# Kernel optimization log

Hardware: AMD Instinct MI355X
Metric: run time of the kernel (lower is better)

## Reference

```python
import jax, jax.numpy as jnp
import numpy as np

NEG_SLOPE = 0.2  # PyG GATv2Conv default negative_slope


def _gatv2(h, src, dst, Wl, bl, Wr, br, att, bias, N):
    """GATv2Conv (concat=True). h: [N,Fin]; att: [H,F]; returns [N,H*F]."""
    H, F = att.shape
    xl = (h @ Wl + bl).reshape(N, H, F)  # source transform
    xr = (h @ Wr + br).reshape(N, H, F)  # target transform
    # per-edge GATv2 score: a^T LeakyReLU(xl[src] + xr[dst])
    e = jax.nn.leaky_relu(xl[src] + xr[dst], negative_slope=NEG_SLOPE)  # [E,H,F]
    logits = jnp.einsum('ehf,hf->eh', e, att)  # [E,H]
    # segment softmax over destination nodes (self-loops guarantee nonempty segments)
    m = jax.ops.segment_max(logits, dst, num_segments=N)  # [N,H]
    p = jnp.exp(logits - m[dst])
    s = jax.ops.segment_sum(p, dst, num_segments=N)  # [N,H]
    alpha = p / s[dst]  # [E,H]
    out = jax.ops.segment_sum(alpha[:, :, None] * xl[src], dst, num_segments=N)  # [N,H,F]
    return out.reshape(N, H * F) + bias


def setup_inputs() -> dict:
    key = jax.random.key(0)
    ks = jax.random.split(key, 16)
    N, E = 30000, 480000
    L, D, H, F = 50, 100, 3, 100
    W = D * H  # 300
    sc = 0.1  # keep activations stable through 5 layers
    return {
        'x': jax.random.randint(ks[0], (N,), 0, L),
        'edge_index': jax.random.randint(ks[1], (2, E), 0, N),
        'emb': jax.random.normal(ks[2], (L, D), jnp.float32),
        'Wl0': jax.random.normal(ks[3], (D, W), jnp.float32) * sc,
        'bl0': jnp.zeros((W,), jnp.float32),
        'Wr0': jax.random.normal(ks[4], (D, W), jnp.float32) * sc,
        'br0': jnp.zeros((W,), jnp.float32),
        'att0': jax.random.normal(ks[5], (H, F), jnp.float32) * sc,
        'bias0': jnp.zeros((W,), jnp.float32),
        'Wl': jax.random.normal(ks[6], (4, W, W), jnp.float32) * sc,
        'bl': jnp.zeros((4, W), jnp.float32),
        'Wr': jax.random.normal(ks[7], (4, W, W), jnp.float32) * sc,
        'br': jnp.zeros((4, W), jnp.float32),
        'att': jax.random.normal(ks[8], (4, H, F), jnp.float32) * sc,
        'bias': jnp.zeros((4, W), jnp.float32),
    }


def reference(x, edge_index, emb, Wl0, bl0, Wr0, br0, att0, bias0,
              Wl, bl, Wr, br, att, bias):
    N = x.shape[0]
    loops = jnp.arange(N)
    src = jnp.concatenate([edge_index[0], loops])  # PyG add_self_loops=True
    dst = jnp.concatenate([edge_index[1], loops])
    h = emb[x]  # node_embedding(x).squeeze()
    h = jax.nn.relu(_gatv2(h, src, dst, Wl0, bl0, Wr0, br0, att0, bias0, N))
    for i in range(4):  # remaining num_gnn_layers-1 convs, each followed by ReLU
        h = jax.nn.relu(_gatv2(h, src, dst, Wl[i], bl[i], Wr[i], br[i], att[i], bias[i], N))
    return h  # [N, heads*hidden] = [N, 300]
```

## Files before the change

kernel.cpp:

```cpp
#include <hip/hip_runtime.h>

#define NODES   30000
#define E0N     480000
#define ETOT    510000
#define D0      100
#define WDIM    300
#define NW      600
#define NEG     0.2f
#define XLP     320

typedef __bf16 bf16x8 __attribute__((ext_vector_type(8)));
typedef float  f32x4  __attribute__((ext_vector_type(4)));

__global__ void count_edges(const int* __restrict__ ei, int* __restrict__ counts) {
    int e = blockIdx.x * 256 + threadIdx.x;
    if (e >= ETOT) return;
    int d = (e < E0N) ? ei[E0N + e] : (e - E0N);
    atomicAdd(&counts[d], 1);
}

__global__ __launch_bounds__(1024) void scan_kernel(const int* __restrict__ counts,
                                                    int* __restrict__ offsets, int n) {
    __shared__ int lds[1024];
    const int CH = 32;
    int t = threadIdx.x;
    int base = t * CH;
    int loc[CH];
    int sum = 0;
    #pragma unroll
    for (int i = 0; i < CH; i++) {
        int v = (base + i < n) ? counts[base + i] : 0;
        loc[i] = sum;
        sum += v;
    }
    lds[t] = sum;
    __syncthreads();
    for (int off = 1; off < 1024; off <<= 1) {
        int v = (t >= off) ? lds[t - off] : 0;
        __syncthreads();
        lds[t] += v;
        __syncthreads();
    }
    int ex = (t == 0) ? 0 : lds[t - 1];
    #pragma unroll
    for (int i = 0; i < CH; i++) {
        int idx = base + i;
        if (idx < n) offsets[idx] = ex + loc[i];
    }
    if (t == 0) offsets[n] = lds[1023];
}

__global__ void scatter_edges(const int* __restrict__ ei, const int* __restrict__ offsets,
                              int* __restrict__ cursor, int* __restrict__ csr_src) {
    int e = blockIdx.x * 256 + threadIdx.x;
    if (e >= ETOT) return;
    int s, d;
    if (e < E0N) { s = ei[e]; d = ei[E0N + e]; }
    else         { s = e - E0N; d = s; }
    int pos = offsets[d] + atomicAdd(&cursor[d], 1);
    csr_src[pos] = s;
}

__device__ __forceinline__ void bfrag_one(const float* Bl, const float* Br,
                                          bf16x8* out, int K, int t) {
    int lane = t & 63;
    int n16  = (t >> 6) % 40;
    int s    = t / (64 * 40);
    int c = n16 * 16 + (lane & 15);
    union { bf16x8 v; __bf16 e[8]; } hi, lo;
    #pragma unroll
    for (int j = 0; j < 8; j++) {
        int k = s * 32 + ((lane >> 4) * 8) + j;
        float x = 0.f;
        if (k < K && c < NW)
            x = (c < WDIM) ? Bl[(size_t)k * WDIM + c] : Br[(size_t)k * WDIM + c - WDIM];
        __bf16 h = (__bf16)x;
        hi.e[j] = h;
        lo.e[j] = (__bf16)(x - (float)h);
    }
    size_t base = ((size_t)(s * 40 + n16) * 2) * 64 + lane;
    out[base]      = hi.v;
    out[base + 64] = lo.v;
}

__global__ void make_bfrag_all(const float* __restrict__ Wl0, const float* __restrict__ Wr0,
                               const float* __restrict__ Wl, const float* __restrict__ Wr,
                               bf16x8* __restrict__ frag0, bf16x8* __restrict__ frag1,
                               size_t fragstride) {
    int t = blockIdx.x * 256 + threadIdx.x;
    const int L0 = 4 * 40 * 64, LN = 10 * 40 * 64;
    if (t < L0) {
        bfrag_one(Wl0, Wr0, frag0, D0, t);
    } else {
        int u = t - L0;
        int layer = u / LN;
        if (layer >= 4) return;
        bfrag_one(Wl + (size_t)layer * WDIM * WDIM, Wr + (size_t)layer * WDIM * WDIM,
                  frag1 + layer * fragstride, WDIM, u - layer * LN);
    }
}

__global__ __launch_bounds__(256) void gemm_mfma(
    const float* __restrict__ A, const int* __restrict__ xmap, int use_map,
    const bf16x8* __restrict__ Bfrag,
    const float* __restrict__ bl, const float* __restrict__ br,
    ushort* __restrict__ Cl16, float* __restrict__ Cr,
    int M, int K, int ksteps) {

    __shared__ bf16x8 Alds[8][2][64];
    __shared__ bf16x8 Blds[8][2][64];

    int id = blockIdx.x;
    int mb = (id & 7) + 8 * (id / 40);
    int cb = (id >> 3) % 5;
    if (mb >= 235) return;

    int tid  = threadIdx.x;
    int lane = tid & 63;
    int wid  = tid >> 6;
    int wm = wid >> 1, wn = wid & 1;
    int row0 = mb * 128;

    f32x4 acc[4][4] = {};

    for (int s = 0; s < ksteps; s++) {
        int kt = s * 32;
        #pragma unroll
        for (int u0 = 0; u0 < 2; u0++) {
            int u = u0 * 256 + tid;
            int m16  = u >> 6;
            int slot = u & 63;
            int kh = slot >> 4, rl = slot & 15;
            int gr = row0 + m16 * 16 + rl;
            int gc = kt + kh * 8;
            float4 v0 = make_float4(0.f,0.f,0.f,0.f), v1 = v0;
            if (gr < M) {
                int ar = use_map ? xmap[gr] : gr;
                const float* ap = A + (size_t)ar * K + gc;
                if (gc + 4 <= K) v0 = *(const float4*)ap;
                if (gc + 8 <= K) v1 = *(const float4*)(ap + 4);
            }
            union { bf16x8 v; __bf16 e[8]; } hi, lo;
            const float* xs0 = (const float*)&v0;
            const float* xs1 = (const float*)&v1;
            #pragma unroll
            for (int j = 0; j < 8; j++) {
                float x = (j < 4) ? xs0[j] : xs1[j - 4];
                __bf16 h = (__bf16)x;
                hi.e[j] = h;
                lo.e[j] = (__bf16)(x - (float)h);
            }
            Alds[m16][0][slot] = hi.v;
            Alds[m16][1][slot] = lo.v;
        }
        {
            const float4* bsrc = (const float4*)(Bfrag + ((size_t)(s * 40 + cb * 8) * 2) * 64);
            float4* bdst = (float4*)&Blds[0][0][0];
            #pragma unroll
            for (int c = 0; c < 4; c++)
                bdst[c * 256 + tid] = bsrc[c * 256 + tid];
        }
        __syncthreads();

        bf16x8 af[4][2], bfr[4][2];
        #pragma unroll
        for (int m = 0; m < 4; m++) {
            af[m][0] = Alds[wm * 4 + m][0][lane];
            af[m][1] = Alds[wm * 4 + m][1][lane];
        }
        #pragma unroll
        for (int n = 0; n < 4; n++) {
            bfr[n][0] = Blds[wn * 4 + n][0][lane];
            bfr[n][1] = Blds[wn * 4 + n][1][lane];
        }
        #pragma unroll
        for (int m = 0; m < 4; m++)
            #pragma unroll
            for (int n = 0; n < 4; n++) {
                acc[m][n] = __builtin_amdgcn_mfma_f32_16x16x32_bf16(af[m][1], bfr[n][0], acc[m][n], 0, 0, 0);
                acc[m][n] = __builtin_amdgcn_mfma_f32_16x16x32_bf16(af[m][0], bfr[n][1], acc[m][n], 0, 0, 0);
                acc[m][n] = __builtin_amdgcn_mfma_f32_16x16x32_bf16(af[m][0], bfr[n][0], acc[m][n], 0, 0, 0);
            }
        __syncthreads();
    }

    int r0 = row0 + wm * 64;
    int c0 = cb * 128 + wn * 64;
    #pragma unroll
    for (int m = 0; m < 4; m++)
        #pragma unroll
        for (int n = 0; n < 4; n++) {
            #pragma unroll
            for (int reg = 0; reg < 4; reg++) {
                int gr = r0 + m * 16 + (lane >> 4) * 4 + reg;
                int gc = c0 + n * 16 + (lane & 15);
                if (gr < M && gc < NW) {
                    if (gc < WDIM) {
                        float v = acc[m][n][reg] + bl[gc];
                        __bf16 b = (__bf16)v;
                        Cl16[(size_t)gr * XLP + gc] = *(ushort*)&b;
                    } else {
                        int cc = gc - WDIM;
                        Cr[(size_t)gr * WDIM + cc] = acc[m][n][reg] + br[cc];
                    }
                }
            }
        }
}

__global__ __launch_bounds__(256) void gat_edge_agg(
    const ushort* __restrict__ xl, const float* __restrict__ xr,
    const int* __restrict__ offsets, const int* __restrict__ csr_src,
    const float* __restrict__ att, const float* __restrict__ bias,
    float* __restrict__ fout) {
    __shared__ float st[4][64][8];
    int wid  = threadIdx.x >> 6;
    int lane = threadIdx.x & 63;
    int node = blockIdx.x * 2 + (wid >> 1);
    int sub  = wid & 1;
    int r = lane & 3;
    bool c0 = lane < 50;
    bool c1 = lane < 36;

    float2 aw2[3], xr2[3];
    const float2* xrrow = (const float2*)(xr + (size_t)node * WDIM);
    #pragma unroll
    for (int j = 0; j < 3; j++) {
        int i = lane + 64 * j;
        if (i < 150) {
            aw2[j].x = att[2 * i]; aw2[j].y = att[2 * i + 1];
            xr2[j] = xrrow[i];
        } else {
            aw2[j].x = 0.f; aw2[j].y = 0.f;
            xr2[j].x = 0.f; xr2[j].y = 0.f;
        }
    }

    float mq = -1e38f, sq = 0.f;
    float2 acc2[3] = {};

    int beg = offsets[node], end = offsets[node + 1];
    int half = (end - beg + 1) >> 1;
    int lo = beg + sub * half;
    int hi = sub ? end : beg + half;

    for (int i = lo; i < hi; i += 2) {
        bool act_b = (i + 1) < hi;
        int sa = csr_src[i];
        int sb = csr_src[act_b ? i + 1 : i];
        const ushort* ra = xl + (size_t)sa * XLP;
        const ushort* rb = xl + (size_t)sb * XLP;
        ushort2 ua[3], ub[3];
        ua[0] = *(const ushort2*)(ra + 2 * lane);
        ub[0] = *(const ushort2*)(rb + 2 * lane);
        ua[1] = *(const ushort2*)(ra + 2 * (lane + 64));
        ub[1] = *(const ushort2*)(rb + 2 * (lane + 64));
        if (lane < 32) {
            ua[2] = *(const ushort2*)(ra + 2 * (lane + 128));
            ub[2] = *(const ushort2*)(rb + 2 * (lane + 128));
        } else { ua[2].x = ua[2].y = ub[2].x = ub[2].y = 0; }

        float2 va[3], vb[3];
        #pragma unroll
        for (int j = 0; j < 3; j++) {
            va[j].x = __uint_as_float(((unsigned)ua[j].x) << 16);
            va[j].y = __uint_as_float(((unsigned)ua[j].y) << 16);
            vb[j].x = __uint_as_float(((unsigned)ub[j].x) << 16);
            vb[j].y = __uint_as_float(((unsigned)ub[j].y) << 16);
        }

        float qa[3], qb[3];
        #pragma unroll
        for (int j = 0; j < 3; j++) {
            float tax = va[j].x + xr2[j].x; tax = fmaxf(tax, NEG * tax);
            float tay = va[j].y + xr2[j].y; tay = fmaxf(tay, NEG * tay);
            float tbx = vb[j].x + xr2[j].x; tbx = fmaxf(tbx, NEG * tbx);
            float tby = vb[j].y + xr2[j].y; tby = fmaxf(tby, NEG * tby);
            qa[j] = tax * aw2[j].x + tay * aw2[j].y;
            qb[j] = tbx * aw2[j].x + tby * aw2[j].y;
        }
        float pa0 = c0 ? qa[0] : 0.f;
        float pa1 = (c0 ? 0.f : qa[0]) + (c1 ? qa[1] : 0.f);
        float pa2 = (c1 ? 0.f : qa[1]) + qa[2];
        float pb0 = c0 ? qb[0] : 0.f;
        float pb1 = (c0 ? 0.f : qb[0]) + (c1 ? qb[1] : 0.f);
        float pb2 = (c1 ? 0.f : qb[1]) + qb[2];

        pa0 += __shfl_xor(pa0, 1, 64); pa1 += __shfl_xor(pa1, 1, 64); pa2 += __shfl_xor(pa2, 1, 64);
        pb0 += __shfl_xor(pb0, 1, 64); pb1 += __shfl_xor(pb1, 1, 64); pb2 += __shfl_xor(pb2, 1, 64);
        pa0 += __shfl_xor(pa0, 2, 64); pa1 += __shfl_xor(pa1, 2, 64); pa2 += __shfl_xor(pa2, 2, 64);
        pb0 += __shfl_xor(pb0, 2, 64); pb1 += __shfl_xor(pb1, 2, 64); pb2 += __shfl_xor(pb2, 2, 64);
        float sqa = (r == 1) ? pa1 : ((r == 2) ? pa2 : pa0);
        float sqb = (r == 1) ? pb1 : ((r == 2) ? pb2 : pb0);
        sqa += __shfl_xor(sqa, 4, 64);  sqb += __shfl_xor(sqb, 4, 64);
        sqa += __shfl_xor(sqa, 8, 64);  sqb += __shfl_xor(sqb, 8, 64);
        sqa += __shfl_xor(sqa, 16, 64); sqb += __shfl_xor(sqb, 16, 64);
        sqa += __shfl_xor(sqa, 32, 64); sqb += __shfl_xor(sqb, 32, 64);
        if (!act_b) sqb = -3e38f;

        float hiq = fmaxf(sqa, sqb);
        if (__any(hiq > mq + 8.f)) {
            float nmq = fmaxf(mq, hiq);
            float eq = __expf(mq - nmq);
            sq *= eq;
            float e0 = __shfl(eq, 0, 64), e1 = __shfl(eq, 1, 64), e2 = __shfl(eq, 2, 64);
            float ej0 = c0 ? e0 : e1, ej1 = c1 ? e1 : e2;
            acc2[0].x *= ej0; acc2[0].y *= ej0;
            acc2[1].x *= ej1; acc2[1].y *= ej1;
            acc2[2].x *= e2;  acc2[2].y *= e2;
            mq = nmq;
        }
        float cqa = __expf(sqa - mq), cqb = __expf(sqb - mq);
        sq += cqa + cqb;
        float ca0 = __shfl(cqa, 0, 64), ca1 = __shfl(cqa, 1, 64), ca2 = __shfl(cqa, 2, 64);
        float cb0 = __shfl(cqb, 0, 64), cb1 = __shfl(cqb, 1, 64), cb2 = __shfl(cqb, 2, 64);
        float caj[3] = { c0 ? ca0 : ca1, c1 ? ca1 : ca2, ca2 };
        float cbj[3] = { c0 ? cb0 : cb1, c1 ? cb1 : cb2, cb2 };
        #pragma unroll
        for (int j = 0; j < 3; j++) {
            acc2[j].x = fmaf(caj[j], va[j].x, acc2[j].x);
            acc2[j].y = fmaf(caj[j], va[j].y, acc2[j].y);
            acc2[j].x = fmaf(cbj[j], vb[j].x, acc2[j].x);
            acc2[j].y = fmaf(cbj[j], vb[j].y, acc2[j].y);
        }
    }

    st[wid][lane][0] = mq;
    st[wid][lane][1] = sq;
    st[wid][lane][2] = acc2[0].x; st[wid][lane][3] = acc2[0].y;
    st[wid][lane][4] = acc2[1].x; st[wid][lane][5] = acc2[1].y;
    st[wid][lane][6] = acc2[2].x; st[wid][lane][7] = acc2[2].y;
    __syncthreads();
    if (sub) return;

    float m1 = st[wid ^ 1][lane][0];
    float s1 = st[wid ^ 1][lane][1];
    float2 o1[3];
    o1[0].x = st[wid ^ 1][lane][2]; o1[0].y = st[wid ^ 1][lane][3];
    o1[1].x = st[wid ^ 1][lane][4]; o1[1].y = st[wid ^ 1][lane][5];
    o1[2].x = st[wid ^ 1][lane][6]; o1[2].y = st[wid ^ 1][lane][7];

    float M  = fmaxf(mq, m1);
    float ea = __expf(mq - M), eb = __expf(m1 - M);
    float sF = sq * ea + s1 * eb;
    float iq = 1.f / sF;
    float ea0 = __shfl(ea, 0, 64), ea1 = __shfl(ea, 1, 64), ea2 = __shfl(ea, 2, 64);
    float eb0 = __shfl(eb, 0, 64), eb1 = __shfl(eb, 1, 64), eb2 = __shfl(eb, 2, 64);
    float i0  = __shfl(iq, 0, 64), i1  = __shfl(iq, 1, 64), i2  = __shfl(iq, 2, 64);
    float eaj[3]  = { c0 ? ea0 : ea1, c1 ? ea1 : ea2, ea2 };
    float ebj[3]  = { c0 ? eb0 : eb1, c1 ? eb1 : eb2, eb2 };
    float isel[3] = { c0 ? i0 : i1,  c1 ? i1 : i2,  i2 };

    #pragma unroll
    for (int j = 0; j < 3; j++) {
        int fi = lane + 64 * j;
        if (fi < 150) {
            float ax = acc2[j].x * eaj[j] + o1[j].x * ebj[j];
            float ay = acc2[j].y * eaj[j] + o1[j].y * ebj[j];
            float2 o;
            o.x = fmaxf(ax * isel[j] + bias[2 * fi],     0.f);
            o.y = fmaxf(ay * isel[j] + bias[2 * fi + 1], 0.f);
            *(float2*)(fout + (size_t)node * WDIM + 2 * fi) = o;
        }
    }
}

static inline size_t align256(size_t x) { return (x + 255) & ~(size_t)255; }

extern "C" void kernel_launch(void* const* d_in, const int* in_sizes, int n_in,
                              void* d_out, int out_size, void* d_ws, size_t ws_size,
                              hipStream_t stream) {
    const int*   x     = (const int*)d_in[0];
    const int*   ei    = (const int*)d_in[1];
    const float* emb   = (const float*)d_in[2];
    const float* Wl0   = (const float*)d_in[3];
    const float* bl0   = (const float*)d_in[4];
    const float* Wr0   = (const float*)d_in[5];
    const float* br0   = (const float*)d_in[6];
    const float* att0  = (const float*)d_in[7];
    const float* bias0 = (const float*)d_in[8];
    const float* Wl    = (const float*)d_in[9];
    const float* bl    = (const float*)d_in[10];
    const float* Wr    = (const float*)d_in[11];
    const float* br    = (const float*)d_in[12];
    const float* att   = (const float*)d_in[13];
    const float* bias  = (const float*)d_in[14];

    char* ws = (char*)d_ws;
    size_t off = 0;
    float* h      = (float*)(ws + off);  off = align256(off + (size_t)NODES * WDIM * 4);
    ushort* xlb16 = (ushort*)(ws + off); off = align256(off + (size_t)NODES * XLP * 2);
    float* xrb    = (float*)(ws + off);  off = align256(off + (size_t)NODES * WDIM * 4);
    int* counts   = (int*)(ws + off);    off = align256(off + (size_t)NODES * 4);
    int* cursor   = (int*)(ws + off);    off = align256(off + (size_t)NODES * 4);
    int* offsets  = (int*)(ws + off);    off = align256(off + (size_t)(NODES + 1) * 4);
    int* csr_src  = (int*)(ws + off);    off = align256(off + (size_t)ETOT * 4);
    size_t frag_l0_elems = (size_t)4 * 40 * 2 * 64;
    size_t frag_ln_elems = (size_t)10 * 40 * 2 * 64;
    bf16x8* bfrag0 = (bf16x8*)(ws + off); off = align256(off + frag_l0_elems * 16);
    bf16x8* bfrag1 = (bf16x8*)(ws + off); off = align256(off + 4 * frag_ln_elems * 16);

    float* out = (float*)d_out;

    {
        int total = 4 * 40 * 64 + 4 * 10 * 40 * 64;
        make_bfrag_all<<<(total + 255) / 256, 256, 0, stream>>>(
            Wl0, Wr0, Wl, Wr, bfrag0, bfrag1, frag_ln_elems);
    }

    hipMemsetAsync(xlb16, 0, (size_t)NODES * XLP * 2, stream);

    hipMemsetAsync(counts, 0, (size_t)NODES * 4, stream);
    hipMemsetAsync(cursor, 0, (size_t)NODES * 4, stream);
    count_edges<<<(ETOT + 255) / 256, 256, 0, stream>>>(ei, counts);
    scan_kernel<<<1, 1024, 0, stream>>>(counts, offsets, NODES);
    scatter_edges<<<(ETOT + 255) / 256, 256, 0, stream>>>(ei, offsets, cursor, csr_src);

    int agg_blocks = NODES / 2;

    gemm_mfma<<<1200, 256, 0, stream>>>(emb, x, 1, bfrag0, bl0, br0, xlb16, xrb, NODES, D0, 4);
    gat_edge_agg<<<agg_blocks, 256, 0, stream>>>(xlb16, xrb, offsets, csr_src, att0, bias0, h);

    for (int i = 0; i < 4; i++) {
        float* dst = (i == 3) ? out : h;
        gemm_mfma<<<1200, 256, 0, stream>>>(h, nullptr, 0, bfrag1 + i * frag_ln_elems,
                                            bl + i * WDIM, br + i * WDIM,
                                            xlb16, xrb, NODES, WDIM, 10);
        gat_edge_agg<<<agg_blocks, 256, 0, stream>>>(xlb16, xrb, offsets, csr_src,
                                                     att + (size_t)i * WDIM,
                                                     bias + (size_t)i * WDIM, dst);
    }
}
```

Measured before the change: 851.5 us.

## Pad xl rows per head and restructure edge aggregation lanes by head

Stores xl in bf16 with each head padded to 128 elements (row pitch 384), so the edge aggregation kernel can map lanes to heads directly: heads 0 and 1 each take half a wave with 4 features per lane, and head 2 takes 2 features per lane. This removes the cross-head select/shuffle logic and the per-edge multi-way shuffles of the softmax coefficients. The GEMM now loads B fragments straight from global memory into registers instead of staging them through LDS. The memset of the xl buffer is dropped, so the padding columns are left uninitialised; padded lanes use zero att weights, but garbage values there could be NaN and leak into the sums. The larger row pitch also adds gather bandwidth.

```diff
diff --git a/kernel.cpp b/kernel.cpp
--- a/kernel.cpp
+++ b/kernel.cpp
@@ -7,7 +7,7 @@
 #define WDIM    300
 #define NW      600
 #define NEG     0.2f
-#define XLP     320
+#define XLP     384
 
 typedef __bf16 bf16x8 __attribute__((ext_vector_type(8)));
 typedef float  f32x4  __attribute__((ext_vector_type(4)));
@@ -108,7 +108,6 @@
     int M, int K, int ksteps) {
 
     __shared__ bf16x8 Alds[8][2][64];
-    __shared__ bf16x8 Blds[8][2][64];
 
     int id = blockIdx.x;
     int mb = (id & 7) + 8 * (id / 40);
@@ -153,25 +152,22 @@
             Alds[m16][0][slot] = hi.v;
             Alds[m16][1][slot] = lo.v;
         }
+        bf16x8 bfr[4][2];
         {
-            const float4* bsrc = (const float4*)(Bfrag + ((size_t)(s * 40 + cb * 8) * 2) * 64);
-            float4* bdst = (float4*)&Blds[0][0][0];
+            const bf16x8* bwave = Bfrag + ((size_t)(s * 40 + cb * 8 + wn * 4) * 2) * 64;
             #pragma unroll
-            for (int c = 0; c < 4; c++)
-                bdst[c * 256 + tid] = bsrc[c * 256 + tid];
+            for (int n = 0; n < 4; n++) {
+                bfr[n][0] = bwave[(n * 2 + 0) * 64 + lane];
+                bfr[n][1] = bwave[(n * 2 + 1) * 64 + lane];
+            }
         }
         __syncthreads();
 
-        bf16x8 af[4][2], bfr[4][2];
+        bf16x8 af[4][2];
         #pragma unroll
         for (int m = 0; m < 4; m++) {
             af[m][0] = Alds[wm * 4 + m][0][lane];
             af[m][1] = Alds[wm * 4 + m][1][lane];
-        }
-        #pragma unroll
-        for (int n = 0; n < 4; n++) {
-            bfr[n][0] = Blds[wn * 4 + n][0][lane];
-            bfr[n][1] = Blds[wn * 4 + n][1][lane];
         }
         #pragma unroll
         for (int m = 0; m < 4; m++)
@@ -197,8 +193,10 @@
                 if (gr < M && gc < NW) {
                     if (gc < WDIM) {
                         float v = acc[m][n][reg] + bl[gc];
+                        int head = gc / 100;
+                        int fh = gc - head * 100;
                         __bf16 b = (__bf16)v;
-                        Cl16[(size_t)gr * XLP + gc] = *(ushort*)&b;
+                        Cl16[(size_t)gr * XLP + head * 128 + fh] = *(ushort*)&b;
                     } else {
                         int cc = gc - WDIM;
                         Cr[(size_t)gr * WDIM + cc] = acc[m][n][reg] + br[cc];
@@ -213,31 +211,30 @@
     const int* __restrict__ offsets, const int* __restrict__ csr_src,
     const float* __restrict__ att, const float* __restrict__ bias,
     float* __restrict__ fout) {
-    __shared__ float st[4][64][8];
+    __shared__ float st[4][64][10];
     int wid  = threadIdx.x >> 6;
     int lane = threadIdx.x & 63;
     int node = blockIdx.x * 2 + (wid >> 1);
     int sub  = wid & 1;
-    int r = lane & 3;
-    bool c0 = lane < 50;
-    bool c1 = lane < 36;
-
-    float2 aw2[3], xr2[3];
-    const float2* xrrow = (const float2*)(xr + (size_t)node * WDIM);
-    #pragma unroll
-    for (int j = 0; j < 3; j++) {
-        int i = lane + 64 * j;
-        if (i < 150) {
-            aw2[j].x = att[2 * i]; aw2[j].y = att[2 * i + 1];
-            xr2[j] = xrrow[i];
-        } else {
-            aw2[j].x = 0.f; aw2[j].y = 0.f;
-            xr2[j].x = 0.f; xr2[j].y = 0.f;
-        }
-    }
-
-    float mq = -1e38f, sq = 0.f;
-    float2 acc2[3] = {};
+    int lq    = lane & 31;
+    int headq = lane >> 5;
+
+    float aw4[4] = {}, xr4[4] = {}, awp[2] = {}, xrp[2] = {};
+    if (lq < 25) {
+        float4 a = *(const float4*)(att + headq * 100 + 4 * lq);
+        float4 b = *(const float4*)(xr + (size_t)node * WDIM + headq * 100 + 4 * lq);
+        aw4[0] = a.x; aw4[1] = a.y; aw4[2] = a.z; aw4[3] = a.w;
+        xr4[0] = b.x; xr4[1] = b.y; xr4[2] = b.z; xr4[3] = b.w;
+    }
+    if (lane < 50) {
+        float2 a = *(const float2*)(att + 200 + 2 * lane);
+        float2 b = *(const float2*)(xr + (size_t)node * WDIM + 200 + 2 * lane);
+        awp[0] = a.x; awp[1] = a.y;
+        xrp[0] = b.x; xrp[1] = b.y;
+    }
+
+    float m_h = -1e38f, s_h = 0.f, m_2 = -1e38f, s_2 = 0.f;
+    float acc4[4] = {}, acc2[2] = {};
 
     int beg = offsets[node], end = offsets[node + 1];
     int half = (end - beg + 1) >> 1;
@@ -250,118 +247,111 @@
         int sb = csr_src[act_b ? i + 1 : i];
         const ushort* ra = xl + (size_t)sa * XLP;
         const ushort* rb = xl + (size_t)sb * XLP;
-        ushort2 ua[3], ub[3];
-        ua[0] = *(const ushort2*)(ra + 2 * lane);
-        ub[0] = *(const ushort2*)(rb + 2 * lane);
-        ua[1] = *(const ushort2*)(ra + 2 * (lane + 64));
-        ub[1] = *(const ushort2*)(rb + 2 * (lane + 64));
-        if (lane < 32) {
-            ua[2] = *(const ushort2*)(ra + 2 * (lane + 128));
-            ub[2] = *(const ushort2*)(rb + 2 * (lane + 128));
-        } else { ua[2].x = ua[2].y = ub[2].x = ub[2].y = 0; }
-
-        float2 va[3], vb[3];
-        #pragma unroll
-        for (int j = 0; j < 3; j++) {
-            va[j].x = __uint_as_float(((unsigned)ua[j].x) << 16);
-            va[j].y = __uint_as_float(((unsigned)ua[j].y) << 16);
-            vb[j].x = __uint_as_float(((unsigned)ub[j].x) << 16);
-            vb[j].y = __uint_as_float(((unsigned)ub[j].y) << 16);
-        }
-
-        float qa[3], qb[3];
-        #pragma unroll
-        for (int j = 0; j < 3; j++) {
-            float tax = va[j].x + xr2[j].x; tax = fmaxf(tax, NEG * tax);
-            float tay = va[j].y + xr2[j].y; tay = fmaxf(tay, NEG * tay);
-            float tbx = vb[j].x + xr2[j].x; tbx = fmaxf(tbx, NEG * tbx);
-            float tby = vb[j].y + xr2[j].y; tby = fmaxf(tby, NEG * tby);
-            qa[j] = tax * aw2[j].x + tay * aw2[j].y;
-            qb[j] = tbx * aw2[j].x + tby * aw2[j].y;
-        }
-        float pa0 = c0 ? qa[0] : 0.f;
-        float pa1 = (c0 ? 0.f : qa[0]) + (c1 ? qa[1] : 0.f);
-        float pa2 = (c1 ? 0.f : qa[1]) + qa[2];
-        float pb0 = c0 ? qb[0] : 0.f;
-        float pb1 = (c0 ? 0.f : qb[0]) + (c1 ? qb[1] : 0.f);
-        float pb2 = (c1 ? 0.f : qb[1]) + qb[2];
-
-        pa0 += __shfl_xor(pa0, 1, 64); pa1 += __shfl_xor(pa1, 1, 64); pa2 += __shfl_xor(pa2, 1, 64);
-        pb0 += __shfl_xor(pb0, 1, 64); pb1 += __shfl_xor(pb1, 1, 64); pb2 += __shfl_xor(pb2, 1, 64);
-        pa0 += __shfl_xor(pa0, 2, 64); pa1 += __shfl_xor(pa1, 2, 64); pa2 += __shfl_xor(pa2, 2, 64);
-        pb0 += __shfl_xor(pb0, 2, 64); pb1 += __shfl_xor(pb1, 2, 64); pb2 += __shfl_xor(pb2, 2, 64);
-        float sqa = (r == 1) ? pa1 : ((r == 2) ? pa2 : pa0);
-        float sqb = (r == 1) ? pb1 : ((r == 2) ? pb2 : pb0);
-        sqa += __shfl_xor(sqa, 4, 64);  sqb += __shfl_xor(sqb, 4, 64);
-        sqa += __shfl_xor(sqa, 8, 64);  sqb += __shfl_xor(sqb, 8, 64);
-        sqa += __shfl_xor(sqa, 16, 64); sqb += __shfl_xor(sqb, 16, 64);
-        sqa += __shfl_xor(sqa, 32, 64); sqb += __shfl_xor(sqb, 32, 64);
-        if (!act_b) sqb = -3e38f;
-
-        float hiq = fmaxf(sqa, sqb);
-        if (__any(hiq > mq + 8.f)) {
-            float nmq = fmaxf(mq, hiq);
-            float eq = __expf(mq - nmq);
-            sq *= eq;
-            float e0 = __shfl(eq, 0, 64), e1 = __shfl(eq, 1, 64), e2 = __shfl(eq, 2, 64);
-            float ej0 = c0 ? e0 : e1, ej1 = c1 ? e1 : e2;
-            acc2[0].x *= ej0; acc2[0].y *= ej0;
-            acc2[1].x *= ej1; acc2[1].y *= ej1;
-            acc2[2].x *= e2;  acc2[2].y *= e2;
-            mq = nmq;
-        }
-        float cqa = __expf(sqa - mq), cqb = __expf(sqb - mq);
-        sq += cqa + cqb;
-        float ca0 = __shfl(cqa, 0, 64), ca1 = __shfl(cqa, 1, 64), ca2 = __shfl(cqa, 2, 64);
-        float cb0 = __shfl(cqb, 0, 64), cb1 = __shfl(cqb, 1, 64), cb2 = __shfl(cqb, 2, 64);
-        float caj[3] = { c0 ? ca0 : ca1, c1 ? ca1 : ca2, ca2 };
-        float cbj[3] = { c0 ? cb0 : cb1, c1 ? cb1 : cb2, cb2 };
-        #pragma unroll
-        for (int j = 0; j < 3; j++) {
-            acc2[j].x = fmaf(caj[j], va[j].x, acc2[j].x);
-            acc2[j].y = fmaf(caj[j], va[j].y, acc2[j].y);
-            acc2[j].x = fmaf(cbj[j], vb[j].x, acc2[j].x);
-            acc2[j].y = fmaf(cbj[j], vb[j].y, acc2[j].y);
-        }
-    }
-
-    st[wid][lane][0] = mq;
-    st[wid][lane][1] = sq;
-    st[wid][lane][2] = acc2[0].x; st[wid][lane][3] = acc2[0].y;
-    st[wid][lane][4] = acc2[1].x; st[wid][lane][5] = acc2[1].y;
-    st[wid][lane][6] = acc2[2].x; st[wid][lane][7] = acc2[2].y;
+        ushort4 a4 = *(const ushort4*)(ra + 4 * lane);
+        ushort4 b4 = *(const ushort4*)(rb + 4 * lane);
+        ushort2 a2 = *(const ushort2*)(ra + 256 + 2 * lane);
+        ushort2 b2 = *(const ushort2*)(rb + 256 + 2 * lane);
+
+        float va4[4], vb4[4], va2[2], vb2[2];
+        va4[0] = __uint_as_float(((unsigned)a4.x) << 16);
+        va4[1] = __uint_as_float(((unsigned)a4.y) << 16);
+        va4[2] = __uint_as_float(((unsigned)a4.z) << 16);
+        va4[3] = __uint_as_float(((unsigned)a4.w) << 16);
+        vb4[0] = __uint_as_float(((unsigned)b4.x) << 16);
+        vb4[1] = __uint_as_float(((unsigned)b4.y) << 16);
+        vb4[2] = __uint_as_float(((unsigned)b4.z) << 16);
+        vb4[3] = __uint_as_float(((unsigned)b4.w) << 16);
+        va2[0] = __uint_as_float(((unsigned)a2.x) << 16);
+        va2[1] = __uint_as_float(((unsigned)a2.y) << 16);
+        vb2[0] = __uint_as_float(((unsigned)b2.x) << 16);
+        vb2[1] = __uint_as_float(((unsigned)b2.y) << 16);
+
+        float qA = 0.f, qB = 0.f, qA2 = 0.f, qB2 = 0.f;
+        #pragma unroll
+        for (int k = 0; k < 4; k++) {
+            float ta = va4[k] + xr4[k]; ta = fmaxf(ta, NEG * ta);
+            float tb = vb4[k] + xr4[k]; tb = fmaxf(tb, NEG * tb);
+            qA = fmaf(ta, aw4[k], qA);
+            qB = fmaf(tb, aw4[k], qB);
+        }
+        #pragma unroll
+        for (int k = 0; k < 2; k++) {
+            float ta = va2[k] + xrp[k]; ta = fmaxf(ta, NEG * ta);
+            float tb = vb2[k] + xrp[k]; tb = fmaxf(tb, NEG * tb);
+            qA2 = fmaf(ta, awp[k], qA2);
+            qB2 = fmaf(tb, awp[k], qB2);
+        }
+        qA += __shfl_xor(qA, 1, 64);  qB += __shfl_xor(qB, 1, 64);
+        qA += __shfl_xor(qA, 2, 64);  qB += __shfl_xor(qB, 2, 64);
+        qA += __shfl_xor(qA, 4, 64);  qB += __shfl_xor(qB, 4, 64);
+        qA += __shfl_xor(qA, 8, 64);  qB += __shfl_xor(qB, 8, 64);
+        qA += __shfl_xor(qA, 16, 64); qB += __shfl_xor(qB, 16, 64);
+        qA2 += __shfl_xor(qA2, 1, 64);  qB2 += __shfl_xor(qB2, 1, 64);
+        qA2 += __shfl_xor(qA2, 2, 64);  qB2 += __shfl_xor(qB2, 2, 64);
+        qA2 += __shfl_xor(qA2, 4, 64);  qB2 += __shfl_xor(qB2, 4, 64);
+        qA2 += __shfl_xor(qA2, 8, 64);  qB2 += __shfl_xor(qB2, 8, 64);
+        qA2 += __shfl_xor(qA2, 16, 64); qB2 += __shfl_xor(qB2, 16, 64);
+        qA2 += __shfl_xor(qA2, 32, 64); qB2 += __shfl_xor(qB2, 32, 64);
+        if (!act_b) { qB = -3e38f; qB2 = -3e38f; }
+
+        float hi_h = fmaxf(qA, qB), hi_2 = fmaxf(qA2, qB2);
+        if (__any(hi_h > m_h + 8.f || hi_2 > m_2 + 8.f)) {
+            float nm_h = fmaxf(m_h, hi_h), nm_2 = fmaxf(m_2, hi_2);
+            float e_h = __expf(m_h - nm_h), e_2 = __expf(m_2 - nm_2);
+            s_h *= e_h; s_2 *= e_2;
+            #pragma unroll
+            for (int k = 0; k < 4; k++) acc4[k] *= e_h;
+            acc2[0] *= e_2; acc2[1] *= e_2;
+            m_h = nm_h; m_2 = nm_2;
+        }
+        float cA  = __expf(qA - m_h),  cB  = __expf(qB - m_h);
+        float cA2 = __expf(qA2 - m_2), cB2 = __expf(qB2 - m_2);
+        s_h += cA + cB; s_2 += cA2 + cB2;
+        #pragma unroll
+        for (int k = 0; k < 4; k++) {
+            acc4[k] = fmaf(cA, va4[k], acc4[k]);
+            acc4[k] = fmaf(cB, vb4[k], acc4[k]);
+        }
+        #pragma unroll
+        for (int k = 0; k < 2; k++) {
+            acc2[k] = fmaf(cA2, va2[k], acc2[k]);
+            acc2[k] = fmaf(cB2, vb2[k], acc2[k]);
+        }
+    }
+
+    st[wid][lane][0] = m_h; st[wid][lane][1] = s_h;
+    st[wid][lane][2] = m_2; st[wid][lane][3] = s_2;
+    st[wid][lane][4] = acc4[0]; st[wid][lane][5] = acc4[1];
+    st[wid][lane][6] = acc4[2]; st[wid][lane][7] = acc4[3];
+    st[wid][lane][8] = acc2[0]; st[wid][lane][9] = acc2[1];
     __syncthreads();
     if (sub) return;
 
-    float m1 = st[wid ^ 1][lane][0];
-    float s1 = st[wid ^ 1][lane][1];
-    float2 o1[3];
-    o1[0].x = st[wid ^ 1][lane][2]; o1[0].y = st[wid ^ 1][lane][3];
-    o1[1].x = st[wid ^ 1][lane][4]; o1[1].y = st[wid ^ 1][lane][5];
-    o1[2].x = st[wid ^ 1][lane][6]; o1[2].y = st[wid ^ 1][lane][7];
-
-    float M  = fmaxf(mq, m1);
-    float ea = __expf(mq - M), eb = __expf(m1 - M);
-    float sF = sq * ea + s1 * eb;
-    float iq = 1.f / sF;
-    float ea0 = __shfl(ea, 0, 64), ea1 = __shfl(ea, 1, 64), ea2 = __shfl(ea, 2, 64);
-    float eb0 = __shfl(eb, 0, 64), eb1 = __shfl(eb, 1, 64), eb2 = __shfl(eb, 2, 64);
-    float i0  = __shfl(iq, 0, 64), i1  = __shfl(iq, 1, 64), i2  = __shfl(iq, 2, 64);
-    float eaj[3]  = { c0 ? ea0 : ea1, c1 ? ea1 : ea2, ea2 };
-    float ebj[3]  = { c0 ? eb0 : eb1, c1 ? eb1 : eb2, eb2 };
-    float isel[3] = { c0 ? i0 : i1,  c1 ? i1 : i2,  i2 };
-
-    #pragma unroll
-    for (int j = 0; j < 3; j++) {
-        int fi = lane + 64 * j;
-        if (fi < 150) {
-            float ax = acc2[j].x * eaj[j] + o1[j].x * ebj[j];
-            float ay = acc2[j].y * eaj[j] + o1[j].y * ebj[j];
-            float2 o;
-            o.x = fmaxf(ax * isel[j] + bias[2 * fi],     0.f);
-            o.y = fmaxf(ay * isel[j] + bias[2 * fi + 1], 0.f);
-            *(float2*)(fout + (size_t)node * WDIM + 2 * fi) = o;
-        }
+    const float* p = st[wid ^ 1][lane];
+    float pm_h = p[0], ps_h = p[1], pm_2 = p[2], ps_2 = p[3];
+
+    float M_h = fmaxf(m_h, pm_h);
+    float ea_h = __expf(m_h - M_h), eb_h = __expf(pm_h - M_h);
+    float inv_h = 1.f / (s_h * ea_h + ps_h * eb_h);
+    float M_2 = fmaxf(m_2, pm_2);
+    float ea_2 = __expf(m_2 - M_2), eb_2 = __expf(pm_2 - M_2);
+    float inv_2 = 1.f / (s_2 * ea_2 + ps_2 * eb_2);
+
+    if (lq < 25) {
+        float4 bv = *(const float4*)(bias + headq * 100 + 4 * lq);
+        float4 o;
+        o.x = fmaxf((acc4[0] * ea_h + p[4] * eb_h) * inv_h + bv.x, 0.f);
+        o.y = fmaxf((acc4[1] * ea_h + p[5] * eb_h) * inv_h + bv.y, 0.f);
+        o.z = fmaxf((acc4[2] * ea_h + p[6] * eb_h) * inv_h + bv.z, 0.f);
+        o.w = fmaxf((acc4[3] * ea_h + p[7] * eb_h) * inv_h + bv.w, 0.f);
+        *(float4*)(fout + (size_t)node * WDIM + headq * 100 + 4 * lq) = o;
+    }
+    if (lane < 50) {
+        float2 bv = *(const float2*)(bias + 200 + 2 * lane);
+        float2 o;
+        o.x = fmaxf((acc2[0] * ea_2 + p[8] * eb_2) * inv_2 + bv.x, 0.f);
+        o.y = fmaxf((acc2[1] * ea_2 + p[9] * eb_2) * inv_2 + bv.y, 0.f);
+        *(float2*)(fout + (size_t)node * WDIM + 200 + 2 * lane) = o;
     }
 }
 
@@ -408,8 +398,6 @@
             Wl0, Wr0, Wl, Wr, bfrag0, bfrag1, frag_ln_elems);
     }
 
-    hipMemsetAsync(xlb16, 0, (size_t)NODES * XLP * 2, stream);
-
     hipMemsetAsync(counts, 0, (size_t)NODES * 4, stream);
     hipMemsetAsync(cursor, 0, (size_t)NODES * 4, stream);
     count_edges<<<(ETOT + 255) / 256, 256, 0, stream>>>(ei, counts);
```

After: 810.5 us. 1.05x faster.
